# Kernel tuning notes

Measured on AMD Instinct MI355X. Metric: run time of the kernel, lower is better.

Reference implementation:

```python
import jax, jax.numpy as jnp
import numpy as np
import math

B, S, H, NH = 2, 1024, 768, 12
DH = H // NH  # 64

def setup_inputs() -> dict:
    key = jax.random.key(0)
    ks = jax.random.split(key, 8)
    sc = 0.02
    return {
        "hidden_states": jax.random.normal(ks[0], (B, S, H), jnp.float32),
        "bbox_pos_emb": jax.random.normal(ks[1], (S, S, B, DH), jnp.float32),
        "attention_mask": jnp.zeros((B, 1, 1, S), jnp.float32),
        "Wq": jax.random.normal(ks[2], (H, H), jnp.float32) * sc,
        "bq": jnp.zeros((H,), jnp.float32),
        "Wk": jax.random.normal(ks[3], (H, H), jnp.float32) * sc,
        "bk": jnp.zeros((H,), jnp.float32),
        "Wv": jax.random.normal(ks[4], (H, H), jnp.float32) * sc,
        "bv": jnp.zeros((H,), jnp.float32),
    }

def reference(hidden_states, bbox_pos_emb, attention_mask, Wq, bq, Wk, bk, Wv, bv):
    b, s, h = hidden_states.shape
    def proj(W, bias):
        # (b, s, h) -> (b, nh, s, dh)
        y = hidden_states @ W.T + bias
        return y.reshape(b, s, NH, DH).transpose(0, 2, 1, 3)
    q = proj(Wq, bq)
    k = proj(Wk, bk)
    v = proj(Wv, bv)
    # QK^T: (b, nh, s, s)
    scores = jnp.einsum("bnid,bnjd->bnij", q, k)
    # bbox bias: (s, s, b, dh) -> (b, s, s, dh); bnid,bijd->bnij
    bbox = bbox_pos_emb.transpose(2, 0, 1, 3)
    scores = scores + jnp.einsum("bnid,bijd->bnij", q, bbox)
    scores = scores / math.sqrt(DH)
    scores = scores + attention_mask
    probs = jax.nn.softmax(scores, axis=-1)
    ctx = jnp.einsum("bnij,bnjd->bnid", probs, v)
    ctx = ctx.transpose(0, 2, 1, 3).reshape(b, s, h)
    return ctx
```

## Files before the change

### kernel.cpp

```cpp
#include <hip/hip_runtime.h>
#include <hip/hip_bf16.h>

typedef short bf4 __attribute__((ext_vector_type(4)));
typedef short short8 __attribute__((ext_vector_type(8)));
typedef float f32x4 __attribute__((ext_vector_type(4)));

#define MFMA(a, b, c) __builtin_amdgcn_mfma_f32_16x16x32_bf16((a), (b), (c), 0, 0, 0)

#define NB 2
#define NS 1024
#define NHID 768
#define NHEAD 12
#define NDH 64

__device__ __forceinline__ short f2bf(float x) {
    __hip_bfloat16 h = __float2bfloat16(x);
    return *reinterpret_cast<short*>(&h);
}

typedef const __attribute__((address_space(1))) void gas_t;
typedef __attribute__((address_space(3))) void las_t;
__device__ __forceinline__ void gld_lds16(const float* g, float* l) {
    __builtin_amdgcn_global_load_lds((gas_t*)g, (las_t*)l, 16, 0, 0);
}
__device__ __forceinline__ void gld_lds16s(const short* g, short* l) {
    __builtin_amdgcn_global_load_lds((gas_t*)g, (las_t*)l, 16, 0, 0);
}

#define NHE (2048 * 768)
#define WE  (768 * 768)
__global__ void cvt_bf16_all(
    const float* __restrict__ hidden,
    const float* __restrict__ Wq, const float* __restrict__ Wk,
    const float* __restrict__ Wv,
    short* __restrict__ Xbf, short* __restrict__ Wbf)
{
    const int base = (blockIdx.x * 256 + threadIdx.x) * 4;
    const float* src; short* dst; int off;
    if (base < NHE)               { src = hidden; dst = Xbf;          off = base; }
    else if (base < NHE + WE)     { src = Wq;     dst = Wbf;          off = base - NHE; }
    else if (base < NHE + 2 * WE) { src = Wk;     dst = Wbf + WE;     off = base - NHE - WE; }
    else                          { src = Wv;     dst = Wbf + 2 * WE; off = base - NHE - 2 * WE; }
    f32x4 v = *reinterpret_cast<const f32x4*>(src + off);
    bf4 r;
    r[0] = f2bf(v[0]); r[1] = f2bf(v[1]); r[2] = f2bf(v[2]); r[3] = f2bf(v[3]);
    *reinterpret_cast<bf4*>(dst + off) = r;
}

__global__ __launch_bounds__(256, 3) void qkv_gemm(
    const short* __restrict__ Xbf, const short* __restrict__ Wbf,
    const float* __restrict__ bq, const float* __restrict__ bk,
    const float* __restrict__ bv,
    short* __restrict__ Qo, short* __restrict__ Ko, short* __restrict__ VTo)
{
    const int lane = threadIdx.x & 63;
    const int wave = threadIdx.x >> 6;
    const int lg = lane >> 4, lr = lane & 15;

    const int m0 = blockIdx.x * 128;
    const int n0 = blockIdx.y * 64;
    const int proj = n0 / NHID;
    const int ncol0 = n0 % NHID;
    const float* bias = proj == 0 ? bq : (proj == 1 ? bk : bv);

    __shared__ short Alds[2][128 * 64];
    __shared__ short Blds[2][64 * 64];

    f32x4 acc[2][4];
    #pragma unroll
    for (int mm = 0; mm < 2; ++mm)
        #pragma unroll
        for (int s = 0; s < 4; ++s) acc[mm][s] = (f32x4){0.f, 0.f, 0.f, 0.f};

    auto stage = [&](int t, int buf) {
        const int k0 = t * 64;
        #pragma unroll
        for (int p = 0; p < 4; ++p) {
            const int op = wave * 4 + p;
            const int unit = op * 64 + lane;
            const int r = unit >> 3, u = unit & 7;
            const int g = u ^ (r & 7);
            gld_lds16s(Xbf + (size_t)(m0 + r) * NHID + k0 + g * 8,
                       &Alds[buf][op * 512]);
        }
        #pragma unroll
        for (int p = 0; p < 2; ++p) {
            const int op = wave * 2 + p;
            const int unit = op * 64 + lane;
            const int r = unit >> 3, u = unit & 7;
            const int g = u ^ (r & 7);
            gld_lds16s(Wbf + (size_t)(n0 + r) * NHID + k0 + g * 8,
                       &Blds[buf][op * 512]);
        }
    };

    auto compute = [&](int buf) {
        #pragma unroll
        for (int kk = 0; kk < 2; ++kk) {
            const int U = kk * 4 + lg;
            short8 a[2];
            #pragma unroll
            for (int mm = 0; mm < 2; ++mm) {
                const int R = wave * 32 + mm * 16 + lr;
                a[mm] = *reinterpret_cast<const short8*>(
                    &Alds[buf][(R * 8 + (U ^ (R & 7))) * 8]);
            }
            #pragma unroll
            for (int s = 0; s < 4; ++s) {
                const int R = s * 16 + lr;
                short8 b = *reinterpret_cast<const short8*>(
                    &Blds[buf][(R * 8 + (U ^ (R & 7))) * 8]);
                acc[0][s] = MFMA(a[0], b, acc[0][s]);
                acc[1][s] = MFMA(a[1], b, acc[1][s]);
            }
        }
    };

    stage(0, 0);
    #pragma unroll 2
    for (int t = 0; t < 12; ++t) {
        const int buf = t & 1;
        asm volatile("s_waitcnt vmcnt(0)" ::: "memory");
        __syncthreads();
        if (t < 11) stage(t + 1, buf ^ 1);
        compute(buf);
    }

    #pragma unroll
    for (int mm = 0; mm < 2; ++mm) {
        #pragma unroll
        for (int s = 0; s < 4; ++s) {
            const int ncol = ncol0 + s * 16 + lr;
            const float badd = bias[ncol];
            #pragma unroll
            for (int r = 0; r < 4; ++r) {
                const int m = m0 + wave * 32 + mm * 16 + lg * 4 + r;
                const short v16 = f2bf(acc[mm][s][r] + badd);
                if (proj == 0) {
                    Qo[(size_t)m * NHID + ncol] = v16;
                } else if (proj == 1) {
                    Ko[(size_t)m * NHID + ncol] = v16;
                } else {
                    const int b = m >> 10, ss = m & 1023;
                    const int h = ncol >> 6, dd = ncol & 63;
                    VTo[(((size_t)(b * NHEAD + h) * NDH + dd) << 10) + ss] = v16;
                }
            }
        }
    }
}

__global__ __launch_bounds__(256, 2) void bias_gemm(
    const short* __restrict__ Q,
    const float* __restrict__ bbox,
    const float* __restrict__ mask,
    short* __restrict__ biasH)
{
    const int lane = threadIdx.x & 63;
    const int wave = threadIdx.x >> 6;
    const int lg = lane >> 4, lr = lane & 15;
    const int i = blockIdx.x;
    const int jq = wave * 256;

    __shared__ float lds[4][2][2048];

    short8 qa[2][2];
    #pragma unroll
    for (int b2 = 0; b2 < 2; ++b2)
        #pragma unroll
        for (int kk = 0; kk < 2; ++kk)
            qa[b2][kk] = *reinterpret_cast<const short8*>(
                Q + ((size_t)(b2 * NS) + i) * NHID + lr * 64 + kk * 32 + lg * 8);

    const int r_half = lane >> 5;
    const int u_lin = lane & 31;

    auto stage = [&](int t, int buf) {
        const int j0 = jq + t * 16;
        float* dst = &lds[wave][buf][0];
        #pragma unroll
        for (int w = 0; w < 8; ++w) {
            const int r = 2 * w + r_half;
            const int u = u_lin ^ (r & 7);
            const float* src = bbox + (size_t)(i * NS + j0 + r) * 128 + u * 4;
            gld_lds16(src, dst + w * 256);
        }
    };

    auto compute = [&](int t, int buf) {
        const float* tile = &lds[wave][buf][0];
        const int j0 = jq + t * 16;
        const int x = lr & 7;
        #pragma unroll
        for (int b2 = 0; b2 < 2; ++b2) {
            const float mk = mask[b2 * NS + j0 + lr];
            f32x4 c = (f32x4){0.f, 0.f, 0.f, 0.f};
            #pragma unroll
            for (int kk = 0; kk < 2; ++kk) {
                const int q0 = b2 * 16 + kk * 8 + lg * 2;
                f32x4 ca = *reinterpret_cast<const f32x4*>(tile + (size_t)(lr * 32 + ((q0)     ^ x)) * 4);
                f32x4 cb = *reinterpret_cast<const f32x4*>(tile + (size_t)(lr * 32 + ((q0 + 1) ^ x)) * 4);
                short8 bf;
                bf[0] = f2bf(ca[0]); bf[1] = f2bf(ca[1]); bf[2] = f2bf(ca[2]); bf[3] = f2bf(ca[3]);
                bf[4] = f2bf(cb[0]); bf[5] = f2bf(cb[1]); bf[6] = f2bf(cb[2]); bf[7] = f2bf(cb[3]);
                c = MFMA(qa[b2][kk], bf, c);
            }
            if (lg < 3) {
                #pragma unroll
                for (int r = 0; r < 4; ++r) {
                    const int n = lg * 4 + r;
                    biasH[((size_t)(b2 * NHEAD + n) * NS + i) * NS + j0 + lr] =
                        f2bf(c[r] * 0.125f + mk);
                }
            }
        }
    };

    stage(0, 0);
    for (int t = 0; t < 16; ++t) {
        const int buf = t & 1;
        asm volatile("s_waitcnt lgkmcnt(0)" ::: "memory");
        if (t < 15) stage(t + 1, buf ^ 1);
        if (t == 0 || t == 15) asm volatile("s_waitcnt vmcnt(8)"  ::: "memory");
        else                   asm volatile("s_waitcnt vmcnt(16)" ::: "memory");
        compute(t, buf);
    }
}

__global__ __launch_bounds__(256, 2) void attn2(
    const short* __restrict__ Q,
    const short* __restrict__ K,
    const short* __restrict__ VT,
    const short* __restrict__ biasH,
    float* __restrict__ out)
{
    const int lane = threadIdx.x & 63;
    const int wave = threadIdx.x >> 6;
    const int lg = lane >> 4, lr = lane & 15;
    const int i0 = blockIdx.x * 16;
    const int bh = blockIdx.y;
    const int b = bh / NHEAD, h = bh % NHEAD;
    const int jq = wave * 256;

    __shared__ short plds[4][16][40];
    __shared__ float numlds[4][16][68];
    __shared__ float denlds[4][16];

    short8 qa[2];
    #pragma unroll
    for (int kk = 0; kk < 2; ++kk)
        qa[kk] = *reinterpret_cast<const short8*>(
            Q + ((size_t)(b * NS) + i0 + lr) * NHID + h * 64 + kk * 32 + lg * 8);

    const short* Kb = K + (size_t)b * NS * NHID + h * 64;
    const short* Vb = VT + (size_t)(b * NHEAD + h) * NDH * NS;
    const short* Bb = biasH + ((size_t)(b * NHEAD + h) * NS + i0) * NS;

    f32x4 ctx[4];
    #pragma unroll
    for (int dt = 0; dt < 4; ++dt) ctx[dt] = (f32x4){0.f, 0.f, 0.f, 0.f};
    f32x4 den = (f32x4){0.f, 0.f, 0.f, 0.f};

    short8 kfA[4], vfA[4]; unsigned short bvA[8];
    short8 kfB[4], vfB[4]; unsigned short bvB[8];

    auto load = [&](int t, short8* kf, short8* vf, unsigned short* bv) {
        const int j0 = jq + t * 32;
        #pragma unroll
        for (int s = 0; s < 2; ++s)
            #pragma unroll
            for (int kk = 0; kk < 2; ++kk)
                kf[s * 2 + kk] = *reinterpret_cast<const short8*>(
                    Kb + (size_t)(j0 + s * 16 + lr) * NHID + kk * 32 + lg * 8);
        #pragma unroll
        for (int dt = 0; dt < 4; ++dt)
            vf[dt] = *reinterpret_cast<const short8*>(
                Vb + (size_t)(dt * 16 + lr) * NS + j0 + lg * 8);
        #pragma unroll
        for (int s = 0; s < 2; ++s)
            #pragma unroll
            for (int r = 0; r < 4; ++r)
                bv[s * 4 + r] = *reinterpret_cast<const unsigned short*>(
                    Bb + (size_t)(lg * 4 + r) * NS + j0 + s * 16 + lr);
    };

    auto compute = [&](const short8* kf, const short8* vf, const unsigned short* bv) {
        f32x4 sc[2];
        #pragma unroll
        for (int s = 0; s < 2; ++s) {
            f32x4 c = (f32x4){0.f, 0.f, 0.f, 0.f};
            c = MFMA(qa[0], kf[s * 2 + 0], c);
            c = MFMA(qa[1], kf[s * 2 + 1], c);
            sc[s] = c;
        }
        #pragma unroll
        for (int s = 0; s < 2; ++s)
            #pragma unroll
            for (int r = 0; r < 4; ++r) {
                const unsigned int u = (unsigned int)bv[s * 4 + r] << 16;
                float bb;
                __builtin_memcpy(&bb, &u, 4);
                sc[s][r] = __expf(sc[s][r] * 0.125f + bb);
            }
        den += sc[0] + sc[1];

        #pragma unroll
        for (int s = 0; s < 2; ++s)
            #pragma unroll
            for (int r = 0; r < 4; ++r)
                plds[wave][lg * 4 + r][s * 16 + lr] = f2bf(sc[s][r]);
        asm volatile("" ::: "memory");
        short8 pa = *reinterpret_cast<const short8*>(&plds[wave][lr][lg * 8]);
        asm volatile("" ::: "memory");

        #pragma unroll
        for (int dt = 0; dt < 4; ++dt) ctx[dt] = MFMA(pa, vf[dt], ctx[dt]);
    };

    load(0, kfA, vfA, bvA);
    #pragma unroll
    for (int tp = 0; tp < 4; ++tp) {
        const int t = tp * 2;
        if (t + 1 < 8) load(t + 1, kfB, vfB, bvB);
        compute(kfA, vfA, bvA);
        if (t + 2 < 8) load(t + 2, kfA, vfA, bvA);
        compute(kfB, vfB, bvB);
    }

    #pragma unroll
    for (int w = 1; w < 16; w <<= 1) {
        f32x4 o;
        #pragma unroll
        for (int r = 0; r < 4; ++r) o[r] = __shfl_xor(den[r], w, 64);
        den += o;
    }

    #pragma unroll
    for (int dt = 0; dt < 4; ++dt)
        #pragma unroll
        for (int r = 0; r < 4; ++r)
            numlds[wave][lg * 4 + r][dt * 16 + lr] = ctx[dt][r];
    if (lr == 0) {
        #pragma unroll
        for (int r = 0; r < 4; ++r) denlds[wave][lg * 4 + r] = den[r];
    }
    __syncthreads();

    const int ti = threadIdx.x >> 4;
    const int tc = (threadIdx.x & 15) * 4;
    f32x4 n = *reinterpret_cast<const f32x4*>(&numlds[0][ti][tc]);
    n += *reinterpret_cast<const f32x4*>(&numlds[1][ti][tc]);
    n += *reinterpret_cast<const f32x4*>(&numlds[2][ti][tc]);
    n += *reinterpret_cast<const f32x4*>(&numlds[3][ti][tc]);
    const float dd = denlds[0][ti] + denlds[1][ti] + denlds[2][ti] + denlds[3][ti];
    const float inv = 1.0f / dd;
    f32x4 o = n * inv;
    *reinterpret_cast<f32x4*>(out + ((size_t)(b * NS) + i0 + ti) * NHID + h * 64 + tc) = o;
}

extern "C" void kernel_launch(void* const* d_in, const int* in_sizes, int n_in,
                              void* d_out, int out_size, void* d_ws, size_t ws_size,
                              hipStream_t stream) {
    (void)in_sizes; (void)n_in; (void)out_size; (void)ws_size;
    const float* hidden = (const float*)d_in[0];
    const float* bbox   = (const float*)d_in[1];
    const float* mask   = (const float*)d_in[2];
    const float* Wq = (const float*)d_in[3]; const float* bq = (const float*)d_in[4];
    const float* Wk = (const float*)d_in[5]; const float* bk = (const float*)d_in[6];
    const float* Wv = (const float*)d_in[7]; const float* bv = (const float*)d_in[8];
    float* out = (float*)d_out;

    char* ws = (char*)d_ws;
    const size_t qkv_bytes = (size_t)NB * NS * NHID * sizeof(short);
    short* Qw  = (short*)ws;
    short* Kw  = (short*)(ws + qkv_bytes);
    short* VTw = (short*)(ws + 2 * qkv_bytes);
    short* biasH = (short*)(ws + 3 * qkv_bytes);
    const size_t bias_bytes = (size_t)NB * NHEAD * NS * NS * sizeof(short);
    short* Xbf = (short*)(ws + 3 * qkv_bytes + bias_bytes);
    short* Wbf = Xbf + (size_t)2048 * NHID;

    const int cvt_total = (NHE + 3 * WE) / 4;
    cvt_bf16_all<<<cvt_total / 256, 256, 0, stream>>>(hidden, Wq, Wk, Wv, Xbf, Wbf);

    dim3 gp(16, 36);
    qkv_gemm<<<gp, 256, 0, stream>>>(Xbf, Wbf, bq, bk, bv, Qw, Kw, VTw);

    bias_gemm<<<NS, 256, 0, stream>>>(Qw, bbox, mask, biasH);

    dim3 ga(NS / 16, NB * NHEAD);
    attn2<<<ga, 256, 0, stream>>>(Qw, Kw, VTw, biasH, out);
}
```

Before: 223.9 us.

## Load attention bias tiles as 16-byte vectors and redistribute through LDS

The attn2 kernel now fetches each 16x32 bf16 bias tile with one 16-byte load per lane instead of eight scattered 2-byte loads. It stages the tile in a per-wave double-buffered LDS region and reads it back in the MFMA accumulator layout. This cuts the number of global memory instructions and improves coalescing on the largest streamed tensor. It also raises the launch-bounds occupancy hint from 2 to 3 blocks, at the cost of extra LDS traffic and footprint and a tighter register budget.

```diff
diff --git a/kernel.cpp b/kernel.cpp
--- a/kernel.cpp
+++ b/kernel.cpp
@@ -227,7 +227,7 @@
     }
 }
 
-__global__ __launch_bounds__(256, 2) void attn2(
+__global__ __launch_bounds__(256, 3) void attn2(
     const short* __restrict__ Q,
     const short* __restrict__ K,
     const short* __restrict__ VT,
@@ -243,6 +243,7 @@
     const int jq = wave * 256;
 
     __shared__ short plds[4][16][40];
+    __shared__ short blds[4][2][16 * 40];
     __shared__ float numlds[4][16][68];
     __shared__ float denlds[4][16];
 
@@ -261,10 +262,10 @@
     for (int dt = 0; dt < 4; ++dt) ctx[dt] = (f32x4){0.f, 0.f, 0.f, 0.f};
     f32x4 den = (f32x4){0.f, 0.f, 0.f, 0.f};
 
-    short8 kfA[4], vfA[4]; unsigned short bvA[8];
-    short8 kfB[4], vfB[4]; unsigned short bvB[8];
-
-    auto load = [&](int t, short8* kf, short8* vf, unsigned short* bv) {
+    short8 kfA[4], vfA[4], bvA;
+    short8 kfB[4], vfB[4], bvB;
+
+    auto load = [&](int t, short8* kf, short8* vf, short8* bv) {
         const int j0 = jq + t * 32;
         #pragma unroll
         for (int s = 0; s < 2; ++s)
@@ -276,15 +277,17 @@
         for (int dt = 0; dt < 4; ++dt)
             vf[dt] = *reinterpret_cast<const short8*>(
                 Vb + (size_t)(dt * 16 + lr) * NS + j0 + lg * 8);
-        #pragma unroll
-        for (int s = 0; s < 2; ++s)
-            #pragma unroll
-            for (int r = 0; r < 4; ++r)
-                bv[s * 4 + r] = *reinterpret_cast<const unsigned short*>(
-                    Bb + (size_t)(lg * 4 + r) * NS + j0 + s * 16 + lr);
-    };
-
-    auto compute = [&](const short8* kf, const short8* vf, const unsigned short* bv) {
+        *bv = *reinterpret_cast<const short8*>(
+            Bb + (size_t)(lane >> 2) * NS + j0 + (lane & 3) * 8);
+    };
+
+    auto storeB = [&](short8 bv, int buf) {
+        *reinterpret_cast<short8*>(
+            &blds[wave][buf][(lane >> 2) * 40 + (lane & 3) * 8]) = bv;
+        asm volatile("" ::: "memory");
+    };
+
+    auto compute = [&](const short8* kf, const short8* vf, int buf) {
         f32x4 sc[2];
         #pragma unroll
         for (int s = 0; s < 2; ++s) {
@@ -297,7 +300,8 @@
         for (int s = 0; s < 2; ++s)
             #pragma unroll
             for (int r = 0; r < 4; ++r) {
-                const unsigned int u = (unsigned int)bv[s * 4 + r] << 16;
+                const unsigned int u = (unsigned int)(unsigned short)
+                    blds[wave][buf][(lg * 4 + r) * 40 + s * 16 + lr] << 16;
                 float bb;
                 __builtin_memcpy(&bb, &u, 4);
                 sc[s][r] = __expf(sc[s][r] * 0.125f + bb);
@@ -317,14 +321,16 @@
         for (int dt = 0; dt < 4; ++dt) ctx[dt] = MFMA(pa, vf[dt], ctx[dt]);
     };
 
-    load(0, kfA, vfA, bvA);
+    load(0, kfA, vfA, &bvA);
     #pragma unroll
     for (int tp = 0; tp < 4; ++tp) {
         const int t = tp * 2;
-        if (t + 1 < 8) load(t + 1, kfB, vfB, bvB);
-        compute(kfA, vfA, bvA);
-        if (t + 2 < 8) load(t + 2, kfA, vfA, bvA);
-        compute(kfB, vfB, bvB);
+        storeB(bvA, 0);
+        if (t + 1 < 8) load(t + 1, kfB, vfB, &bvB);
+        compute(kfA, vfA, 0);
+        storeB(bvB, 1);
+        if (t + 2 < 8) load(t + 2, kfA, vfA, &bvA);
+        compute(kfB, vfB, 1);
     }
 
     #pragma unroll
```

Result: no change. 223.0 us (-0.4%).
